# Kernel optimization log

Hardware: AMD Instinct MI355X
Metric: run time of the kernel (lower is better)

The kernel has to match this reference:

```python
import jax, jax.numpy as jnp
import numpy as np

B, L, D_MODEL, HEADS, EXP, DEPTH = 2, 2048, 1024, 16, 2, 12
D_EXP = D_MODEL * EXP
D_HEAD = D_EXP // HEADS


def _layernorm(x, g, b, eps=1e-5):
    mu = jnp.mean(x, axis=-1, keepdims=True)
    var = jnp.mean(jnp.square(x - mu), axis=-1, keepdims=True)
    return (x - mu) * jax.lax.rsqrt(var + eps) * g + b


def setup_inputs() -> dict:
    key = jax.random.key(0)
    ks = jax.random.split(key, 4)
    x = jax.random.normal(ks[0], (B, L, D_MODEL), dtype=jnp.float32)
    w_in = jax.random.normal(ks[1], (D_MODEL, 4 * D_EXP), dtype=jnp.float32) * 0.02
    w_out = jax.random.normal(ks[2], (D_EXP, D_MODEL), dtype=jnp.float32) * (0.02 / np.sqrt(2 * DEPTH))
    return {
        "x": x,
        "ln1_g": jnp.ones((D_MODEL,), jnp.float32),
        "ln1_b": jnp.zeros((D_MODEL,), jnp.float32),
        "ln2_g": jnp.ones((D_MODEL,), jnp.float32),
        "ln2_b": jnp.zeros((D_MODEL,), jnp.float32),
        "w_in": w_in,
        "w_out": w_out,
        "smear_factor": jnp.linspace(-6.0, 6.0, HEADS, dtype=jnp.float32),
        "log_scale": jnp.zeros((HEADS,), jnp.float32),
    }


def reference(x, ln1_g, ln1_b, ln2_g, ln2_b, w_in, w_out, smear_factor, log_scale):
    b, l, d = x.shape
    h = smear_factor.shape[0]
    d_exp = w_in.shape[1] // 4
    dh = d_exp // h

    qkvp = _layernorm(x, ln1_g, ln1_b) @ w_in  # [b, l, 4*d_exp]
    q, k, v, p = jnp.split(qkvp, 4, axis=-1)
    # 'b i (h d) -> b h i d'
    to_heads = lambda t: t.reshape(b, l, h, dh).transpose(0, 2, 1, 3)
    q, k, v = to_heads(q), to_heads(k), to_heads(v)

    # smeared keys: k_i <- (1-s)*k_i + s*k_{i-1}  (zero at i=0)
    smear = jax.nn.sigmoid(smear_factor)[None, :, None, None]
    k_prev = jnp.pad(k, ((0, 0), (0, 0), (1, 0), (0, 0)))[:, :, :-1, :]
    k = (1.0 - smear) * k + smear * k_prev

    # ALiBi-style additive mask: slope[h]*j on causal part, -1e10 above diag
    half = h // 2
    slopes = jnp.concatenate([2.0 ** jnp.linspace(0.0, -8.0, half), jnp.zeros((h - half,), jnp.float32)])
    j = jnp.arange(l)
    causal = jnp.where(j[None, :] > j[:, None], jnp.float32(-1e10), jnp.float32(0.0))  # [l, l]
    mask = slopes[:, None, None] * j[None, None, :].astype(jnp.float32) + causal[None, :, :]  # [h, l, l]

    # SDPA with q/s, k/s and default scale 1/sqrt(dh): logits = q k^T / (s^2 sqrt(dh))
    inv = 1.0 / (jnp.exp(2.0 * log_scale)[None, :, None, None] * jnp.sqrt(jnp.float32(dh)))
    logits = jnp.einsum('bhid,bhjd->bhij', q, k) * inv + mask[None]
    attn = jax.nn.softmax(logits, axis=-1)
    o = jnp.einsum('bhij,bhjd->bhid', attn, v)
    o = o.transpose(0, 2, 1, 3).reshape(b, l, h * dh)  # 'b h i d -> b i (h d)'

    out = (jax.nn.silu(p) * o) @ w_out
    return _layernorm(out, ln2_g, ln2_b)
```

## Files before the change

kernel.cpp:

```cpp
#include <hip/hip_runtime.h>

typedef unsigned short u16;
typedef __attribute__((ext_vector_type(8))) short bf16x8;
typedef __attribute__((ext_vector_type(8))) unsigned short u16x8;
typedef __attribute__((ext_vector_type(4))) float f32x4;

#define L_SEQ 2048
#define NTOK 4096
#define DMODEL 1024
#define DEXP 2048
#define NH 16
#define DH 128

__device__ __forceinline__ u16 f2bf(float f) {
    unsigned u = __float_as_uint(f);
    unsigned r = (u + 0x7FFFu + ((u >> 16) & 1u)) >> 16;
    return (u16)r;
}
__device__ __forceinline__ float bf2f(u16 h) {
    return __uint_as_float(((unsigned)h) << 16);
}

template <int CTRL>
__device__ __forceinline__ float dpp_f(float x) {
    return __int_as_float(__builtin_amdgcn_update_dpp(0, __float_as_int(x), CTRL, 0xF, 0xF, true));
}
__device__ __forceinline__ float red16_max(float x) {
    x = fmaxf(x, dpp_f<0xB1>(x));
    x = fmaxf(x, dpp_f<0x4E>(x));
    x = fmaxf(x, dpp_f<0x124>(x));
    x = fmaxf(x, dpp_f<0x128>(x));
    return x;
}

__device__ __forceinline__ void gl_lds16(const u16* g, u16* l) {
    __builtin_amdgcn_global_load_lds((const __attribute__((address_space(1))) void*)g,
                                     (__attribute__((address_space(3))) void*)l, 16, 0, 0);
}

__global__ void conv_transpose(const float* __restrict__ in, u16* __restrict__ out, int R, int C) {
    __shared__ unsigned tile[32][33];
    int c0 = blockIdx.x * 32, r0 = blockIdx.y * 32;
    int tx = threadIdx.x, ty = threadIdx.y;
    for (int j = 0; j < 32; j += 8)
        tile[ty + j][tx] = (unsigned)f2bf(in[(size_t)(r0 + ty + j) * C + c0 + tx]);
    __syncthreads();
    for (int j = 0; j < 32; j += 8)
        out[(size_t)(c0 + ty + j) * R + r0 + tx] = (u16)tile[tx][ty + j];
}

__global__ __launch_bounds__(256) void ln_fwd(const float* __restrict__ x, const float* __restrict__ g,
                                              const float* __restrict__ bta, void* __restrict__ outp,
                                              int out_bf16) {
    int row = blockIdx.x;
    int t = threadIdx.x;
    const float* xr = x + (size_t)row * DMODEL;
    float4 xv = *(const float4*)&xr[t * 4];
    float s = xv.x + xv.y + xv.z + xv.w;
    float s2 = xv.x * xv.x + xv.y * xv.y + xv.z * xv.z + xv.w * xv.w;
    for (int off = 32; off >= 1; off >>= 1) {
        s += __shfl_xor(s, off);
        s2 += __shfl_xor(s2, off);
    }
    __shared__ float red[10];
    int w = t >> 6;
    if ((t & 63) == 0) { red[w] = s; red[4 + w] = s2; }
    __syncthreads();
    if (t == 0) {
        red[8] = red[0] + red[1] + red[2] + red[3];
        red[9] = red[4] + red[5] + red[6] + red[7];
    }
    __syncthreads();
    float mu = red[8] * (1.0f / DMODEL);
    float var = red[9] * (1.0f / DMODEL) - mu * mu;
    float rstd = rsqrtf(var + 1e-5f);
    float vals[4] = {xv.x, xv.y, xv.z, xv.w};
    for (int e = 0; e < 4; e++) {
        int c = t * 4 + e;
        float y = (vals[e] - mu) * rstd * g[c] + bta[c];
        if (out_bf16) ((u16*)outp)[(size_t)row * DMODEL + c] = f2bf(y);
        else          ((float*)outp)[(size_t)row * DMODEL + c] = y;
    }
}

__device__ __forceinline__ void store_out(u16* C, size_t idx, float v) { C[idx] = f2bf(v); }
__device__ __forceinline__ void store_out(float* C, size_t idx, float v) { C[idx] = v; }

template <typename OutT>
__global__ __launch_bounds__(256) void gemm_bt(const u16* __restrict__ A, const u16* __restrict__ BT,
                                               OutT* __restrict__ C, int M, int N, int K) {
    __shared__ u16 a_s[4096];
    __shared__ u16 b_s[4096];
    int tid = threadIdx.x;
    unsigned NX = gridDim.x;
    unsigned lin = blockIdx.x + NX * blockIdx.y;
    unsigned per = NX >> 3;
    unsigned xcd = lin & 7, t = lin >> 3;
    unsigned n_p = xcd * per + (t % per);
    unsigned m_p = t / per;
    int m0 = m_p * 128, n0 = n_p * 128;
    int w = tid >> 6, lane = tid & 63, quad = lane >> 4, ln = lane & 15;
    int wr = (w >> 1) * 64, wc = (w & 1) * 64;
    f32x4 zero4 = {0.f, 0.f, 0.f, 0.f};
    f32x4 acc[4][4];
    for (int r = 0; r < 4; r++)
        for (int c = 0; c < 4; c++) acc[r][c] = zero4;

    int lrow = lane >> 2, lseg = (lane & 3) * 8;
    const u16* Ag0 = A + (size_t)(m0 + 32 * w + lrow) * K + lseg;
    const u16* Ag1 = Ag0 + (size_t)16 * K;
    const u16* Bg0 = BT + (size_t)(n0 + 32 * w + lrow) * K + lseg;
    const u16* Bg1 = Bg0 + (size_t)16 * K;
    u16* al0 = &a_s[(2 * w) * 512];
    u16* al1 = &a_s[(2 * w + 1) * 512];
    u16* bl0 = &b_s[(2 * w) * 512];
    u16* bl1 = &b_s[(2 * w + 1) * 512];

    for (int k0 = 0; k0 < K; k0 += 32) {
        __syncthreads();
        gl_lds16(Ag0 + k0, al0);
        gl_lds16(Ag1 + k0, al1);
        gl_lds16(Bg0 + k0, bl0);
        gl_lds16(Bg1 + k0, bl1);
        __syncthreads();
        bf16x8 af[4], bfr[4];
        for (int r = 0; r < 4; r++) af[r]  = *(const bf16x8*)&a_s[(wr + r * 16 + ln) * 32 + quad * 8];
        for (int c = 0; c < 4; c++) bfr[c] = *(const bf16x8*)&b_s[(wc + c * 16 + ln) * 32 + quad * 8];
        for (int r = 0; r < 4; r++)
            for (int c = 0; c < 4; c++)
                acc[r][c] = __builtin_amdgcn_mfma_f32_16x16x32_bf16(af[r], bfr[c], acc[r][c], 0, 0, 0);
    }
    for (int r = 0; r < 4; r++)
        for (int c = 0; c < 4; c++)
            for (int e = 0; e < 4; e++) {
                int row = m0 + wr + r * 16 + quad * 4 + e;
                int col = n0 + wc + c * 16 + ln;
                store_out(C, (size_t)row * N + col, acc[r][c][e]);
            }
}

__global__ __launch_bounds__(256) void smear_kernel(const u16* __restrict__ qkvp,
                                                    const float* __restrict__ smear_f,
                                                    u16* __restrict__ k_sm) {
    int gid = blockIdx.x * 256 + threadIdx.x;
    int base = gid * 8;
    int bl = base >> 11;
    int c = base & 2047;
    int h = c >> 7;
    int d = c & 127;
    int l = bl & (L_SEQ - 1);
    int bb = bl >> 11;
    float s = 1.0f / (1.0f + __expf(-smear_f[h]));
    u16x8 cur = *(const u16x8*)&qkvp[(size_t)bl * 8192 + 2048 + c];
    u16x8 prv = {0, 0, 0, 0, 0, 0, 0, 0};
    if (l > 0) prv = *(const u16x8*)&qkvp[(size_t)(bl - 1) * 8192 + 2048 + c];
    u16x8 outv;
    for (int u = 0; u < 8; u++) {
        float kc = bf2f(cur[u]);
        float kp = bf2f(prv[u]);
        outv[u] = f2bf((1.0f - s) * kc + s * kp);
    }
    *(u16x8*)&k_sm[(((size_t)(bb * 16 + h)) * L_SEQ + l) * DH + d] = outv;
}

__global__ void vT_kernel(const u16* __restrict__ qkvp, u16* __restrict__ v_t) {
    __shared__ unsigned tile[32][33];
    int l0 = blockIdx.x * 32, d0 = blockIdx.y * 32;
    int bh = blockIdx.z;
    int bb = bh >> 4, h = bh & 15;
    int tx = threadIdx.x, ty = threadIdx.y;
    size_t tokb = (size_t)bb * L_SEQ;
    for (int j = 0; j < 32; j += 8)
        tile[ty + j][tx] = (unsigned)qkvp[(tokb + l0 + ty + j) * 8192 + 4096 + h * DH + d0 + tx];
    __syncthreads();
    for (int j = 0; j < 32; j += 8)
        v_t[((size_t)bh * DH + d0 + ty + j) * L_SEQ + l0 + tx] = (u16)tile[tx][ty + j];
}

__global__ __launch_bounds__(256) void attn_kernel(const u16* __restrict__ qkvp,
                                                   const u16* __restrict__ k_sm,
                                                   const u16* __restrict__ v_t,
                                                   u16* __restrict__ ag2,
                                                   const float* __restrict__ log_scale) {
    __shared__ u16 k_s[16384];
    __shared__ u16 vt_s[16384];
    __shared__ u16 p_s[4608];
    int tid = threadIdx.x;
    unsigned lin = blockIdx.x + 16u * blockIdx.y;
    unsigned xcd = lin & 7, tt = lin >> 3;
    int bh = (int)(xcd * 4 + (tt & 3));
    int pair = (int)(tt >> 2);
    int bb = bh >> 4, h = bh & 15;
    int w = tid >> 6, lane = tid & 63, quad = lane >> 4, ln = lane & 15;
    size_t tokb = (size_t)bb * L_SEQ;

    const float LOG2E = 1.44269504f;
    float inv = 1.0f / (__expf(2.0f * log_scale[h]) * sqrtf((float)DH));
    float scl = inv * LOG2E;
    float slope2 = ((h < 8) ? exp2f(-8.0f * (float)h / 7.0f) : 0.0f) * LOG2E;

    int lrow = lane >> 2, lcol = lane & 3;
    int lsw8 = (lcol ^ ((lrow >> 1) & 3)) * 8;
    int qsw = (quad ^ ((ln >> 1) & 3)) * 8;
    f32x4 zero4 = {0.f, 0.f, 0.f, 0.f};
    u16* pw = &p_s[w * 1152];
    const short ONE_BF = (short)0x3F80;
    bf16x8 ones = {ONE_BF, ONE_BF, ONE_BF, ONE_BF, ONE_BF, ONE_BF, ONE_BF, ONE_BF};

    for (int sidx = 0; sidx < 2; sidx++) {
        int ib = sidx == 0 ? (31 - pair) : pair;
        int i0 = ib * 64;
        int si = i0 + w * 16;

        bf16x8 qf[4];
        for (int kt = 0; kt < 4; kt++)
            qf[kt] = *(const bf16x8*)&qkvp[(tokb + si + ln) * 8192 + h * DH + kt * 32 + quad * 8];

        float m_i[4];
        for (int r = 0; r < 4; r++) m_i[r] = -1e30f;
        f32x4 o_acc[8], l_acc;
        for (int dt = 0; dt < 8; dt++) o_acc[dt] = zero4;
        l_acc = zero4;

        const u16* kg[4];
        for (int g = 0; g < 4; g++)
            kg[g] = k_sm + ((size_t)bh * L_SEQ + g * 16 + lrow) * DH + w * 32 + lsw8;
        const u16* vg[4];
        int vloff[4];
        for (int q = 0; q < 4; q++) {
            int c = w * 4 + q;
            int jt = c >> 3, dg = c & 7;
            vg[q] = v_t + ((size_t)bh * DH + dg * 16 + lrow) * L_SEQ + jt * 32 + lsw8;
            vloff[q] = jt * 4096 + dg * 512;
        }

        for (int g = 0; g < 4; g++) { gl_lds16(kg[g], &k_s[w * 2048 + g * 512]); kg[g] += 64 * DH; }
        for (int q = 0; q < 4; q++) { gl_lds16(vg[q], &vt_s[vloff[q]]); vg[q] += 64; }
        __syncthreads();

        int cur = 0;
        for (int j0 = 0; j0 <= i0; j0 += 64) {
            if (j0 + 64 <= i0) {
                int nb = (cur ^ 1) * 8192;
                for (int g = 0; g < 4; g++) { gl_lds16(kg[g], &k_s[nb + w * 2048 + g * 512]); kg[g] += 64 * DH; }
                for (int q = 0; q < 4; q++) { gl_lds16(vg[q], &vt_s[nb + vloff[q]]); vg[q] += 64; }
            }
            const u16* kb = &k_s[cur * 8192];
            const u16* vb = &vt_s[cur * 8192];

            f32x4 sc[4];
            for (int ct = 0; ct < 4; ct++) sc[ct] = zero4;
            __builtin_amdgcn_s_setprio(1);
            for (int kt = 0; kt < 4; kt++)
                for (int ct = 0; ct < 4; ct++) {
                    bf16x8 bfr = *(const bf16x8*)&kb[kt * 2048 + (ct * 16 + ln) * 32 + qsw];
                    sc[ct] = __builtin_amdgcn_mfma_f32_16x16x32_bf16(qf[kt], bfr, sc[ct], 0, 0, 0);
                }
            __builtin_amdgcn_s_setprio(0);

            bool full = (j0 + 63 <= si);
            float s2[4][4];
            float aj0 = slope2 * (float)(j0 + ln);
            for (int ct = 0; ct < 4; ct++) {
                float ajv = aj0 + slope2 * (float)(16 * ct);
                int j = j0 + ct * 16 + ln;
                for (int r = 0; r < 4; r++) {
                    float v = fmaf(sc[ct][r], scl, ajv);
                    if (!full) {
                        int i = si + quad * 4 + r;
                        if (j > i) v = -3.0e38f;
                    }
                    s2[ct][r] = v;
                }
            }
            float pm[4];
            bool need = false;
            for (int r = 0; r < 4; r++) {
                float mr = fmaxf(fmaxf(s2[0][r], s2[1][r]), fmaxf(s2[2][r], s2[3][r]));
                mr = red16_max(mr);
                pm[r] = mr;
                need |= (mr - m_i[r] > 8.0f);
            }
            if (__any(need)) {
                float alpha[4];
                for (int r = 0; r < 4; r++) {
                    float mnew = fmaxf(m_i[r], pm[r]);
                    alpha[r] = exp2f(m_i[r] - mnew);
                    m_i[r] = mnew;
                }
                for (int dt = 0; dt < 8; dt++) {
                    f32x4 o = o_acc[dt];
                    for (int r = 0; r < 4; r++) o[r] *= alpha[r];
                    o_acc[dt] = o;
                }
                for (int r = 0; r < 4; r++) l_acc[r] *= alpha[r];
            }
            for (int r = 0; r < 4; r++) {
                for (int ct = 0; ct < 4; ct++) {
                    float p = exp2f(s2[ct][r] - m_i[r]);
                    u16 pb = (u16)(__float_as_uint(p) >> 16);
                    pw[(quad * 4 + r) * 72 + ct * 16 + ln] = pb;
                }
            }
            asm volatile("s_waitcnt lgkmcnt(0)" ::: "memory");
            __builtin_amdgcn_s_setprio(1);
            for (int ks = 0; ks < 2; ks++) {
                bf16x8 pa = *(const bf16x8*)&pw[ln * 72 + ks * 32 + quad * 8];
                l_acc = __builtin_amdgcn_mfma_f32_16x16x32_bf16(pa, ones, l_acc, 0, 0, 0);
                for (int dt = 0; dt < 8; dt++) {
                    bf16x8 vf = *(const bf16x8*)&vb[ks * 4096 + (dt * 16 + ln) * 32 + qsw];
                    o_acc[dt] = __builtin_amdgcn_mfma_f32_16x16x32_bf16(pa, vf, o_acc[dt], 0, 0, 0);
                }
            }
            __builtin_amdgcn_s_setprio(0);
            __syncthreads();
            cur ^= 1;
        }

        float rinv[4];
        for (int r = 0; r < 4; r++) rinv[r] = __builtin_amdgcn_rcpf(l_acc[r]);
        for (int dt = 0; dt < 8; dt++)
            for (int r = 0; r < 4; r++) {
                int i = si + quad * 4 + r;
                int dcol = dt * 16 + ln;
                float o = o_acc[dt][r] * rinv[r];
                float pv = bf2f(qkvp[(tokb + i) * 8192 + 6144 + h * DH + dcol]);
                float gate = pv * __builtin_amdgcn_rcpf(1.0f + exp2f(-pv * LOG2E));
                ag2[(tokb + i) * 2048 + h * DH + dcol] = f2bf(gate * o);
            }
    }
}

extern "C" void kernel_launch(void* const* d_in, const int* in_sizes, int n_in,
                              void* d_out, int out_size, void* d_ws, size_t ws_size,
                              hipStream_t stream) {
    const float* x       = (const float*)d_in[0];
    const float* ln1_g   = (const float*)d_in[1];
    const float* ln1_b   = (const float*)d_in[2];
    const float* ln2_g   = (const float*)d_in[3];
    const float* ln2_b   = (const float*)d_in[4];
    const float* w_in    = (const float*)d_in[5];
    const float* w_out   = (const float*)d_in[6];
    const float* smear_f = (const float*)d_in[7];
    const float* logsc   = (const float*)d_in[8];
    float* out = (float*)d_out;
    char* ws = (char*)d_ws;

    u16* w_inT   = (u16*)(ws + 0);
    u16* w_outT  = (u16*)(ws + (size_t)16777216);
    u16* lnA     = (u16*)(ws + (size_t)20971520);
    u16* qkvp    = (u16*)(ws + (size_t)29360128);
    u16* k_sm    = (u16*)(ws + (size_t)96468992);
    u16* ag2     = (u16*)(ws + (size_t)113246208);
    float* out_pre = (float*)(ws + (size_t)96468992);
    u16* v_t     = (u16*)(ws + 0);

    dim3 b32x8(32, 8);
    conv_transpose<<<dim3(8192 / 32, 1024 / 32), b32x8, 0, stream>>>(w_in, w_inT, 1024, 8192);
    conv_transpose<<<dim3(1024 / 32, 2048 / 32), b32x8, 0, stream>>>(w_out, w_outT, 2048, 1024);
    ln_fwd<<<NTOK, 256, 0, stream>>>(x, ln1_g, ln1_b, (void*)lnA, 1);
    gemm_bt<u16><<<dim3(8192 / 128, 4096 / 128), 256, 0, stream>>>(lnA, w_inT, qkvp, NTOK, 8192, 1024);
    smear_kernel<<<4096, 256, 0, stream>>>(qkvp, smear_f, k_sm);
    vT_kernel<<<dim3(L_SEQ / 32, DH / 32, 32), b32x8, 0, stream>>>(qkvp, v_t);
    attn_kernel<<<dim3(16, 32), 256, 0, stream>>>(qkvp, k_sm, v_t, ag2, logsc);
    gemm_bt<float><<<dim3(1024 / 128, 4096 / 128), 256, 0, stream>>>(ag2, w_outT, out_pre, NTOK, 1024, 2048);
    ln_fwd<<<NTOK, 256, 0, stream>>>(out_pre, ln2_g, ln2_b, (void*)out, 0);
}
```

Baseline: 379.3 us.

## Double-buffer GEMM LDS tiles and always rescale in attention softmax

The GEMM kernel now uses two LDS buffers, prefetching the next K tile while MFMAs run on the current one. This replaces two barriers per iteration with one and raises wave priority around the MFMA block. The attention online softmax drops the lazy threshold-based rescale (only when the max grew by more than 8) and rescales whenever the max changes, computing probabilities against the new max in the same loop. That costs more frequent rescaling of the output accumulators but removes the separate pass.

```diff
diff --git a/kernel.cpp b/kernel.cpp
--- a/kernel.cpp
+++ b/kernel.cpp
@@ -89,8 +89,8 @@
 template <typename OutT>
 __global__ __launch_bounds__(256) void gemm_bt(const u16* __restrict__ A, const u16* __restrict__ BT,
                                                OutT* __restrict__ C, int M, int N, int K) {
-    __shared__ u16 a_s[4096];
-    __shared__ u16 b_s[4096];
+    __shared__ u16 a_s[2][4096];
+    __shared__ u16 b_s[2][4096];
     int tid = threadIdx.x;
     unsigned NX = gridDim.x;
     unsigned lin = blockIdx.x + NX * blockIdx.y;
@@ -111,24 +111,33 @@
     const u16* Ag1 = Ag0 + (size_t)16 * K;
     const u16* Bg0 = BT + (size_t)(n0 + 32 * w + lrow) * K + lseg;
     const u16* Bg1 = Bg0 + (size_t)16 * K;
-    u16* al0 = &a_s[(2 * w) * 512];
-    u16* al1 = &a_s[(2 * w + 1) * 512];
-    u16* bl0 = &b_s[(2 * w) * 512];
-    u16* bl1 = &b_s[(2 * w + 1) * 512];
-
+    int lo0 = (2 * w) * 512, lo1 = (2 * w + 1) * 512;
+
+    gl_lds16(Ag0, &a_s[0][lo0]);
+    gl_lds16(Ag1, &a_s[0][lo1]);
+    gl_lds16(Bg0, &b_s[0][lo0]);
+    gl_lds16(Bg1, &b_s[0][lo1]);
+    __syncthreads();
+
+    int cur = 0;
     for (int k0 = 0; k0 < K; k0 += 32) {
-        __syncthreads();
-        gl_lds16(Ag0 + k0, al0);
-        gl_lds16(Ag1 + k0, al1);
-        gl_lds16(Bg0 + k0, bl0);
-        gl_lds16(Bg1 + k0, bl1);
-        __syncthreads();
+        if (k0 + 32 < K) {
+            int nb = cur ^ 1;
+            gl_lds16(Ag0 + k0 + 32, &a_s[nb][lo0]);
+            gl_lds16(Ag1 + k0 + 32, &a_s[nb][lo1]);
+            gl_lds16(Bg0 + k0 + 32, &b_s[nb][lo0]);
+            gl_lds16(Bg1 + k0 + 32, &b_s[nb][lo1]);
+        }
         bf16x8 af[4], bfr[4];
-        for (int r = 0; r < 4; r++) af[r]  = *(const bf16x8*)&a_s[(wr + r * 16 + ln) * 32 + quad * 8];
-        for (int c = 0; c < 4; c++) bfr[c] = *(const bf16x8*)&b_s[(wc + c * 16 + ln) * 32 + quad * 8];
+        for (int r = 0; r < 4; r++) af[r]  = *(const bf16x8*)&a_s[cur][(wr + r * 16 + ln) * 32 + quad * 8];
+        for (int c = 0; c < 4; c++) bfr[c] = *(const bf16x8*)&b_s[cur][(wc + c * 16 + ln) * 32 + quad * 8];
+        __builtin_amdgcn_s_setprio(1);
         for (int r = 0; r < 4; r++)
             for (int c = 0; c < 4; c++)
                 acc[r][c] = __builtin_amdgcn_mfma_f32_16x16x32_bf16(af[r], bfr[c], acc[r][c], 0, 0, 0);
+        __builtin_amdgcn_s_setprio(0);
+        __syncthreads();
+        cur ^= 1;
     }
     for (int r = 0; r < 4; r++)
         for (int c = 0; c < 4; c++)
@@ -273,34 +282,28 @@
                     s2[ct][r] = v;
                 }
             }
-            float pm[4];
-            bool need = false;
+            float alpha[4];
+            bool any_resc = false;
             for (int r = 0; r < 4; r++) {
                 float mr = fmaxf(fmaxf(s2[0][r], s2[1][r]), fmaxf(s2[2][r], s2[3][r]));
                 mr = red16_max(mr);
-                pm[r] = mr;
-                need |= (mr - m_i[r] > 8.0f);
-            }
-            if (__any(need)) {
-                float alpha[4];
-                for (int r = 0; r < 4; r++) {
-                    float mnew = fmaxf(m_i[r], pm[r]);
-                    alpha[r] = exp2f(m_i[r] - mnew);
-                    m_i[r] = mnew;
-                }
+                float mnew = fmaxf(m_i[r], mr);
+                alpha[r] = exp2f(m_i[r] - mnew);
+                any_resc |= (alpha[r] != 1.0f);
+                m_i[r] = mnew;
+                for (int ct = 0; ct < 4; ct++) {
+                    float p = exp2f(s2[ct][r] - mnew);
+                    u16 pb = (u16)(__float_as_uint(p) >> 16);
+                    pw[(quad * 4 + r) * 72 + ct * 16 + ln] = pb;
+                }
+            }
+            if (__any(any_resc)) {
                 for (int dt = 0; dt < 8; dt++) {
                     f32x4 o = o_acc[dt];
                     for (int r = 0; r < 4; r++) o[r] *= alpha[r];
                     o_acc[dt] = o;
                 }
                 for (int r = 0; r < 4; r++) l_acc[r] *= alpha[r];
-            }
-            for (int r = 0; r < 4; r++) {
-                for (int ct = 0; ct < 4; ct++) {
-                    float p = exp2f(s2[ct][r] - m_i[r]);
-                    u16 pb = (u16)(__float_as_uint(p) >> 16);
-                    pw[(quad * 4 + r) * 72 + ct * 16 + ln] = pb;
-                }
             }
             asm volatile("s_waitcnt lgkmcnt(0)" ::: "memory");
             __builtin_amdgcn_s_setprio(1);
```

Result: faster. 363.9 us (-4.0%).
